# Optimization experiments

Hardware: AMD Instinct MI355X
Metric: run time of the kernel (lower is better)

The kernel has to match this reference:

```python
import jax, jax.numpy as jnp
import numpy as np
from jax import lax

EPS = 1e-8


def setup_inputs() -> dict:
    key = jax.random.key(0)
    k1, k2, k3, k4, k5 = jax.random.split(key, 5)
    b, c_in, c_out, h, w_sp, k, z = 8, 256, 256, 128, 128, 3, 512
    return {
        "x": jax.random.normal(k1, (b, c_in, h, w_sp), dtype=jnp.float32),
        "w": jax.random.normal(k2, (b, z), dtype=jnp.float32),
        "weight": jax.random.normal(k3, (c_out, c_in, k, k), dtype=jnp.float32),
        "affine_w": jax.random.normal(k4, (c_in, z), dtype=jnp.float32) * 0.02,
        "affine_b": jax.random.normal(k5, (c_in,), dtype=jnp.float32) * 0.02,
    }


def reference(x, w, weight, affine_w, affine_b):
    # style: [b, c_in] -> broadcast over (out_ch, kh, kw); +1 as in StyleGAN2
    style = w @ affine_w.T + affine_b + 1.0                      # [b, c_in]
    wgt = weight[None] * style[:, None, :, None, None]           # [b, O, I, kh, kw]
    # demodulation
    denom = lax.rsqrt(jnp.sum(wgt * wgt, axis=(2, 3, 4)) + EPS)  # [b, O]
    wgt = wgt * denom[:, :, None, None, None]

    # per-sample conv (equivalent to groups=b grouped conv), 'same' padding
    def conv_one(xi, wi):
        # xi: [I, H, W], wi: [O, I, kh, kw]
        return lax.conv_general_dilated(
            xi[None], wi, window_strides=(1, 1), padding="SAME",
            dimension_numbers=("NCHW", "OIHW", "NCHW"))[0]

    return jax.vmap(conv_one)(x, wgt)                            # [b, O, H, W]
```

## Files before the change

### kernel.cpp

```cpp
#include <hip/hip_runtime.h>
#include <hip/hip_bf16.h>

#define EPS 1e-8f

using short8 = __attribute__((ext_vector_type(8))) short;
using f32x16 = __attribute__((ext_vector_type(16))) float;
typedef unsigned short u16;

#define BARRIER() do { __builtin_amdgcn_s_barrier(); \
                       asm volatile("" ::: "memory"); } while (0)
#define LGKM0() asm volatile("s_waitcnt lgkmcnt(0)" ::: "memory")

__device__ __forceinline__ u16 f2bf(float f) {
    union { float f; unsigned u; } v; v.f = f;
    unsigned u = v.u;
    return (u16)((u + 0x7FFFu + ((u >> 16) & 1u)) >> 16);
}

__device__ __forceinline__ int swz(int s) {
    return (s & ~7) | ((s + (s >> 3)) & 7);
}

__global__ void style_kernel(const float* __restrict__ w,
                             const float* __restrict__ affine_w,
                             const float* __restrict__ affine_b,
                             float* __restrict__ style) {
    int b = blockIdx.x;
    int i = threadIdx.x;
    __shared__ float wb[512];
    for (int z = threadIdx.x; z < 512; z += 256) wb[z] = w[b * 512 + z];
    __syncthreads();
    const float* aw = affine_w + i * 512;
    float acc = 0.f;
#pragma unroll 4
    for (int z = 0; z < 512; z += 4) {
        float4 a4 = *reinterpret_cast<const float4*>(aw + z);
        acc += a4.x * wb[z] + a4.y * wb[z + 1] + a4.z * wb[z + 2] + a4.w * wb[z + 3];
    }
    style[b * 256 + i] = acc + affine_b[i] + 1.0f;
}

__global__ void modw_kernel(const float* __restrict__ weight,
                            const float* __restrict__ style,
                            u16* __restrict__ wgt) {
    int b = blockIdx.x >> 8;
    int o = blockIdx.x & 255;
    int ic = threadIdx.x;
    float s = style[b * 256 + ic];
    const float* wp = weight + (size_t)(o * 256 + ic) * 9;
    float m[9];
    float ss = 0.f;
#pragma unroll
    for (int t = 0; t < 9; ++t) { m[t] = wp[t] * s; ss += m[t] * m[t]; }
#pragma unroll
    for (int off = 32; off > 0; off >>= 1) ss += __shfl_down(ss, off);
    __shared__ float part[4];
    int lane = threadIdx.x & 63, wid = threadIdx.x >> 6;
    if (lane == 0) part[wid] = ss;
    __syncthreads();
    float denom = rsqrtf(part[0] + part[1] + part[2] + part[3] + EPS);
    int g = ic >> 3, j = ic & 7;
#pragma unroll
    for (int t = 0; t < 9; ++t) {
        size_t idx = ((((size_t)(b * 9 + t) * 32 + g) * 256 + o) << 3) + j;
        wgt[idx] = f2bf(m[t] * denom);
    }
}

__global__ __launch_bounds__(256, 2) void conv_kernel(
    const float* __restrict__ x,
    const u16* __restrict__ wgt,
    float* __restrict__ out) {

    __shared__ __align__(16) u16 Xs[2][4][4][130][8];

    int bid = blockIdx.x;
    int swzb = (bid & 7) * 128 + (bid >> 3);
    int ht = swzb & 63, ot = (swzb >> 6) & 1, b = swzb >> 7;
    int h0 = ht * 2;

    int tid = threadIdx.x, lane = tid & 63, wid = tid >> 6;
    int wm = wid >> 1, wr = wid & 1;
    int l31 = lane & 31, lh = lane >> 5;
    int lw = lane & 31, hi = lane >> 5;
    int jbase = hi * 4;
    int koff = hi * 2;

    int hr = h0 + wid - 1;
    bool hValid = ((unsigned)hr < 128u);
    int hc = hValid ? hr : 0;

    const u16* aBase = wgt + ((size_t)(b * 9) * 32 * 256 +
                              (size_t)(lh * 256 + ot * 128 + wm * 64 + l31)) * 8;
    const float* xSt = x + (((size_t)(b * 256 + jbase)) * 128 + hc) * 128 + 4 * lw;

    auto loadA = [&](short8 dst[2][2], int c, int t) {
#pragma unroll
        for (int kk = 0; kk < 2; ++kk)
#pragma unroll
            for (int mi = 0; mi < 2; ++mi)
                dst[kk][mi] = *reinterpret_cast<const short8*>(
                    aBase + (size_t)(((t * 32) + c * 4 + kk * 2) * 256 + mi * 32) * 8);
    };
    auto issueX = [&](float* dst, int c1, int g) {
        const float* sp = xSt + (size_t)(c1 * 32 + g * 8) * 16384;
#pragma unroll
        for (int i = 0; i < 4; ++i)
            *reinterpret_cast<float4*>(&dst[i * 4]) =
                *reinterpret_cast<const float4*>(sp + (size_t)i * 16384);
    };
    auto writeX = [&](const float* src, int g, int bx) {
        unsigned X[4][2];
#pragma unroll
        for (int k = 0; k < 4; ++k)
#pragma unroll
            for (int d = 0; d < 2; ++d) {
                __hip_bfloat16 b0 = __float2bfloat16(src[(2 * d) * 4 + k]);
                __hip_bfloat16 b1 = __float2bfloat16(src[(2 * d + 1) * 4 + k]);
                X[k][d] = (unsigned)reinterpret_cast<u16&>(b0) |
                          ((unsigned)reinterpret_cast<u16&>(b1) << 16);
            }
        unsigned a00 = X[0][0], c00 = X[2][0];
        unsigned a01 = X[0][1], c01 = X[2][1];
        unsigned a10 = X[1][0], c10 = X[3][0];
        unsigned a11 = X[1][1], c11 = X[3][1];
        asm("v_permlane32_swap_b32 %0, %1" : "+v"(a00), "+v"(c00));
        asm("v_permlane32_swap_b32 %0, %1" : "+v"(a01), "+v"(c01));
        asm("v_permlane32_swap_b32 %0, %1" : "+v"(a10), "+v"(c10));
        asm("v_permlane32_swap_b32 %0, %1" : "+v"(a11), "+v"(c11));
        union { unsigned d[4]; short8 v; } oA, oB;
        oA.d[0] = a00; oA.d[1] = a01; oA.d[2] = c00; oA.d[3] = c01;
        oB.d[0] = a10; oB.d[1] = a11; oB.d[2] = c10; oB.d[3] = c11;
        int slotA = 1 + 4 * lw + koff;
        *reinterpret_cast<short8*>(&Xs[bx][wid][g][swz(slotA)][0])     = oA.v;
        *reinterpret_cast<short8*>(&Xs[bx][wid][g][swz(slotA + 1)][0]) = oB.v;
    };

    {
        short8 z = {0, 0, 0, 0, 0, 0, 0, 0};
        short8* p0 = reinterpret_cast<short8*>(&Xs[0][0][0][0][0]);
        for (int i = tid; i < 4160; i += 256) p0[i] = z;
    }
    __syncthreads();

    short8 afC[2][2], afN[2][2];
    if (hValid) {
        float xg0[16];
#pragma unroll
        for (int g = 0; g < 4; ++g) { issueX(xg0, 0, g); writeX(xg0, g, 0); }
    }
    loadA(afC, 0, 0);
    LGKM0();
    BARRIER();

    f32x16 acc[2][4] = {};
    float xg[16];

    for (int c = 0; c < 8; ++c) {
        int buf = c & 1;
        bool stage = (c < 7) && hValid;
#pragma unroll
        for (int t = 0; t < 9; ++t) {
            bool lastTap = (c == 7 && t == 8);
            if (!lastTap)
                loadA(afN, t < 8 ? c : c + 1, t < 8 ? t + 1 : 0);
            if (stage) {
                if (t >= 1 && t < 5) writeX(xg, t - 1, buf ^ 1);
                if (t < 4)           issueX(xg, c + 1, t);
            }

            int kh = t / 3, kw = t - kh * 3;
            int pr[4];
#pragma unroll
            for (int ni = 0; ni < 4; ++ni) pr[ni] = swz(ni * 32 + l31 + kw);
            short8 bx8[2][4];
#pragma unroll
            for (int kk = 0; kk < 2; ++kk)
#pragma unroll
                for (int ni = 0; ni < 4; ++ni)
                    bx8[kk][ni] = *reinterpret_cast<const short8*>(
                        &Xs[buf][wr + kh][kk * 2 + lh][pr[ni]][0]);
#pragma unroll
            for (int mi = 0; mi < 2; ++mi)
#pragma unroll
                for (int ni = 0; ni < 4; ++ni)
#pragma unroll
                    for (int kk = 0; kk < 2; ++kk)
                        acc[mi][ni] = __builtin_amdgcn_mfma_f32_32x32x16_bf16(
                            afC[kk][mi], bx8[kk][ni], acc[mi][ni], 0, 0, 0);

            if (!lastTap) {
#pragma unroll
                for (int k2 = 0; k2 < 2; ++k2)
#pragma unroll
                    for (int mi = 0; mi < 2; ++mi)
                        afC[k2][mi] = afN[k2][mi];
            }
        }
        if (c < 7) { LGKM0(); BARRIER(); }
    }

    int h = h0 + wr;
#pragma unroll
    for (int mi = 0; mi < 2; ++mi) {
        int ob = ot * 128 + wm * 64 + mi * 32 + 4 * lh;
#pragma unroll
        for (int ni = 0; ni < 4; ++ni) {
            int w_ = ni * 32 + l31;
#pragma unroll
            for (int reg = 0; reg < 16; ++reg) {
                int o = ob + (reg & 3) + 8 * (reg >> 2);
                out[(((size_t)(b * 256 + o) * 128 + h) * 128) + w_] = acc[mi][ni][reg];
            }
        }
    }
}

extern "C" void kernel_launch(void* const* d_in, const int* in_sizes, int n_in,
                              void* d_out, int out_size, void* d_ws, size_t ws_size,
                              hipStream_t stream) {
    const float* x        = (const float*)d_in[0];
    const float* w        = (const float*)d_in[1];
    const float* weight   = (const float*)d_in[2];
    const float* affine_w = (const float*)d_in[3];
    const float* affine_b = (const float*)d_in[4];
    float* out = (float*)d_out;

    float* style = (float*)d_ws;
    u16* wgt = (u16*)((char*)d_ws + 8192);

    style_kernel<<<8, 256, 0, stream>>>(w, affine_w, affine_b, style);
    modw_kernel<<<2048, 256, 0, stream>>>(weight, style, wgt);
    conv_kernel<<<1024, 256, 0, stream>>>(x, wgt, out);
}
```

Before: 168.4 us.

## Enlarge conv tile to four output rows per block with 512 threads

```diff
diff --git a/kernel.cpp b/kernel.cpp
--- a/kernel.cpp
+++ b/kernel.cpp
@@ -67,32 +67,27 @@
     }
 }
 
-__global__ __launch_bounds__(256, 2) void conv_kernel(
+__global__ __launch_bounds__(512, 2) void conv_kernel(
     const float* __restrict__ x,
     const u16* __restrict__ wgt,
     float* __restrict__ out) {
 
-    __shared__ __align__(16) u16 Xs[2][4][4][130][8];
+    __shared__ __align__(16) u16 Xs[2][6][4][130][8];
 
     int bid = blockIdx.x;
-    int swzb = (bid & 7) * 128 + (bid >> 3);
-    int ht = swzb & 63, ot = (swzb >> 6) & 1, b = swzb >> 7;
-    int h0 = ht * 2;
+    int swzb = (bid & 7) * 64 + (bid >> 3);
+    int ht = swzb & 31, ot = (swzb >> 5) & 1, b = swzb >> 6;
+    int h0 = ht * 4;
 
     int tid = threadIdx.x, lane = tid & 63, wid = tid >> 6;
-    int wm = wid >> 1, wr = wid & 1;
+    int wm = wid >> 2, wr = wid & 3;
     int l31 = lane & 31, lh = lane >> 5;
     int lw = lane & 31, hi = lane >> 5;
     int jbase = hi * 4;
     int koff = hi * 2;
 
-    int hr = h0 + wid - 1;
-    bool hValid = ((unsigned)hr < 128u);
-    int hc = hValid ? hr : 0;
-
     const u16* aBase = wgt + ((size_t)(b * 9) * 32 * 256 +
                               (size_t)(lh * 256 + ot * 128 + wm * 64 + l31)) * 8;
-    const float* xSt = x + (((size_t)(b * 256 + jbase)) * 128 + hc) * 128 + 4 * lw;
 
     auto loadA = [&](short8 dst[2][2], int c, int t) {
 #pragma unroll
@@ -102,52 +97,61 @@
                 dst[kk][mi] = *reinterpret_cast<const short8*>(
                     aBase + (size_t)(((t * 32) + c * 4 + kk * 2) * 256 + mi * 32) * 8);
     };
-    auto issueX = [&](float* dst, int c1, int g) {
-        const float* sp = xSt + (size_t)(c1 * 32 + g * 8) * 16384;
-#pragma unroll
-        for (int i = 0; i < 4; ++i)
-            *reinterpret_cast<float4*>(&dst[i * 4]) =
-                *reinterpret_cast<const float4*>(sp + (size_t)i * 16384);
+    auto issueX = [&](float* dst, int c1, int u) {
+        int row = u >> 2, g = u & 3;
+        int hr = h0 + row - 1;
+        if ((unsigned)hr < 128u) {
+            const float* sp = x +
+                ((size_t)(b * 256 + c1 * 32 + g * 8 + jbase) * 128 + hr) * 128 + 4 * lw;
+#pragma unroll
+            for (int i = 0; i < 4; ++i)
+                *reinterpret_cast<float4*>(&dst[i * 4]) =
+                    *reinterpret_cast<const float4*>(sp + (size_t)i * 16384);
+        }
     };
-    auto writeX = [&](const float* src, int g, int bx) {
-        unsigned X[4][2];
-#pragma unroll
-        for (int k = 0; k < 4; ++k)
-#pragma unroll
-            for (int d = 0; d < 2; ++d) {
-                __hip_bfloat16 b0 = __float2bfloat16(src[(2 * d) * 4 + k]);
-                __hip_bfloat16 b1 = __float2bfloat16(src[(2 * d + 1) * 4 + k]);
-                X[k][d] = (unsigned)reinterpret_cast<u16&>(b0) |
-                          ((unsigned)reinterpret_cast<u16&>(b1) << 16);
-            }
-        unsigned a00 = X[0][0], c00 = X[2][0];
-        unsigned a01 = X[0][1], c01 = X[2][1];
-        unsigned a10 = X[1][0], c10 = X[3][0];
-        unsigned a11 = X[1][1], c11 = X[3][1];
-        asm("v_permlane32_swap_b32 %0, %1" : "+v"(a00), "+v"(c00));
-        asm("v_permlane32_swap_b32 %0, %1" : "+v"(a01), "+v"(c01));
-        asm("v_permlane32_swap_b32 %0, %1" : "+v"(a10), "+v"(c10));
-        asm("v_permlane32_swap_b32 %0, %1" : "+v"(a11), "+v"(c11));
-        union { unsigned d[4]; short8 v; } oA, oB;
-        oA.d[0] = a00; oA.d[1] = a01; oA.d[2] = c00; oA.d[3] = c01;
-        oB.d[0] = a10; oB.d[1] = a11; oB.d[2] = c10; oB.d[3] = c11;
-        int slotA = 1 + 4 * lw + koff;
-        *reinterpret_cast<short8*>(&Xs[bx][wid][g][swz(slotA)][0])     = oA.v;
-        *reinterpret_cast<short8*>(&Xs[bx][wid][g][swz(slotA + 1)][0]) = oB.v;
+    auto writeX = [&](const float* src, int u, int bx) {
+        int row = u >> 2, g = u & 3;
+        int hr = h0 + row - 1;
+        if ((unsigned)hr < 128u) {
+            unsigned X[4][2];
+#pragma unroll
+            for (int k = 0; k < 4; ++k)
+#pragma unroll
+                for (int d = 0; d < 2; ++d) {
+                    __hip_bfloat16 b0 = __float2bfloat16(src[(2 * d) * 4 + k]);
+                    __hip_bfloat16 b1 = __float2bfloat16(src[(2 * d + 1) * 4 + k]);
+                    X[k][d] = (unsigned)reinterpret_cast<u16&>(b0) |
+                              ((unsigned)reinterpret_cast<u16&>(b1) << 16);
+                }
+            unsigned a00 = X[0][0], c00 = X[2][0];
+            unsigned a01 = X[0][1], c01 = X[2][1];
+            unsigned a10 = X[1][0], c10 = X[3][0];
+            unsigned a11 = X[1][1], c11 = X[3][1];
+            asm("v_permlane32_swap_b32 %0, %1" : "+v"(a00), "+v"(c00));
+            asm("v_permlane32_swap_b32 %0, %1" : "+v"(a01), "+v"(c01));
+            asm("v_permlane32_swap_b32 %0, %1" : "+v"(a10), "+v"(c10));
+            asm("v_permlane32_swap_b32 %0, %1" : "+v"(a11), "+v"(c11));
+            union { unsigned d[4]; short8 v; } oA, oB;
+            oA.d[0] = a00; oA.d[1] = a01; oA.d[2] = c00; oA.d[3] = c01;
+            oB.d[0] = a10; oB.d[1] = a11; oB.d[2] = c10; oB.d[3] = c11;
+            int slotA = 1 + 4 * lw + koff;
+            *reinterpret_cast<short8*>(&Xs[bx][row][g][swz(slotA)][0])     = oA.v;
+            *reinterpret_cast<short8*>(&Xs[bx][row][g][swz(slotA + 1)][0]) = oB.v;
+        }
     };
 
     {
         short8 z = {0, 0, 0, 0, 0, 0, 0, 0};
         short8* p0 = reinterpret_cast<short8*>(&Xs[0][0][0][0][0]);
-        for (int i = tid; i < 4160; i += 256) p0[i] = z;
+        for (int i = tid; i < 6240; i += 512) p0[i] = z;
     }
     __syncthreads();
 
     short8 afC[2][2], afN[2][2];
-    if (hValid) {
+    {
         float xg0[16];
 #pragma unroll
-        for (int g = 0; g < 4; ++g) { issueX(xg0, 0, g); writeX(xg0, g, 0); }
+        for (int k = 0; k < 3; ++k) { issueX(xg0, 0, wid * 3 + k); writeX(xg0, wid * 3 + k, 0); }
     }
     loadA(afC, 0, 0);
     LGKM0();
@@ -158,15 +162,15 @@
 
     for (int c = 0; c < 8; ++c) {
         int buf = c & 1;
-        bool stage = (c < 7) && hValid;
+        bool stage = (c < 7);
 #pragma unroll
         for (int t = 0; t < 9; ++t) {
             bool lastTap = (c == 7 && t == 8);
             if (!lastTap)
                 loadA(afN, t < 8 ? c : c + 1, t < 8 ? t + 1 : 0);
             if (stage) {
-                if (t >= 1 && t < 5) writeX(xg, t - 1, buf ^ 1);
-                if (t < 4)           issueX(xg, c + 1, t);
+                if (t >= 1 && t < 4) writeX(xg, wid * 3 + (t - 1), buf ^ 1);
+                if (t < 3)           issueX(xg, c + 1, wid * 3 + t);
             }
 
             int kh = t / 3, kw = t - kh * 3;
@@ -231,5 +235,5 @@
 
     style_kernel<<<8, 256, 0, stream>>>(w, affine_w, affine_b, style);
     modw_kernel<<<2048, 256, 0, stream>>>(weight, style, wgt);
-    conv_kernel<<<1024, 256, 0, stream>>>(x, wgt, out);
-}
+    conv_kernel<<<512, 512, 0, stream>>>(x, wgt, out);
+}
```

Measured after the change: 175.7 us. 4.3% more time.
